# Kernel optimization log

Measured on AMD Instinct MI355X. Metric: run time of the kernel, lower is better.

The kernel has to match this reference:

```python
import jax, jax.numpy as jnp
import numpy as np

# DeformConv (v1, mmcv-style) config
N, C, H, W = 4, 64, 128, 128
OUT_C, KH, KW = 64, 3, 3
STRIDE, PAD, DIL, DG = 1, 1, 1, 1  # groups = 1


def setup_inputs() -> dict:
    key = jax.random.key(0)
    k1, k2, k3 = jax.random.split(key, 3)
    x = jax.random.normal(k1, (N, C, H, W), dtype=jnp.float32)
    offset = jax.random.normal(k2, (N, 2 * DG * KH * KW, H, W), dtype=jnp.float32)
    n_fan = C * KH * KW
    std = 1.0 / np.sqrt(n_fan)
    weight = jax.random.uniform(k3, (OUT_C, C, KH, KW), minval=-std, maxval=std, dtype=jnp.float32)
    return {"input_tensor": x, "offset": offset, "weight": weight}


def _deform_conv(x, offset, weight, stride, padding, dilation, dg):
    n, c, h, w = x.shape
    o, cin_g, kh, kw = weight.shape
    k = kh * kw
    ho = (h + 2 * padding - dilation * (kh - 1) - 1) // stride + 1
    wo = (w + 2 * padding - dilation * (kw - 1) - 1) // stride + 1

    # offset layout: [n, dg*k*2, ho, wo] with (dy, dx) pairs per kernel point
    off = offset.reshape(n, dg, k, 2, ho, wo)
    dy, dx = off[:, :, :, 0], off[:, :, :, 1]  # [n, dg, k, ho, wo]

    ky, kx = jnp.meshgrid(jnp.arange(kh), jnp.arange(kw), indexing="ij")
    ky = ky.reshape(k).astype(x.dtype)
    kx = kx.reshape(k).astype(x.dtype)

    base_y = (jnp.arange(ho) * stride - padding).astype(x.dtype)
    base_x = (jnp.arange(wo) * stride - padding).astype(x.dtype)
    # sampling positions [n, dg, k, ho, wo]
    py = base_y[None, None, None, :, None] + (ky * dilation)[None, None, :, None, None] + dy
    px = base_x[None, None, None, None, :] + (kx * dilation)[None, None, :, None, None] + dx

    cg = c // dg
    xg = x.reshape(n, dg, cg, h * w)

    y0 = jnp.floor(py)
    x0 = jnp.floor(px)
    ly = py - y0  # bilinear weights
    lx = px - x0
    y0i = y0.astype(jnp.int32)
    x0i = x0.astype(jnp.int32)

    def gather(yi, xi):
        # zero contribution for out-of-bounds neighbors (matches mmcv bilinear)
        valid = (yi >= 0) & (yi < h) & (xi >= 0) & (xi < w)
        idx = jnp.clip(yi, 0, h - 1) * w + jnp.clip(xi, 0, w - 1)  # [n, dg, k, ho, wo]
        v = jnp.take_along_axis(xg, idx.reshape(n, dg, 1, -1), axis=3)  # [n, dg, cg, k*ho*wo]
        v = v.reshape(n, dg, cg, k, ho, wo)
        return v * valid[:, :, None].astype(x.dtype)

    v00 = gather(y0i, x0i)
    v01 = gather(y0i, x0i + 1)
    v10 = gather(y0i + 1, x0i)
    v11 = gather(y0i + 1, x0i + 1)

    wy = ly[:, :, None]  # [n, dg, 1, k, ho, wo]
    wx = lx[:, :, None]
    sampled = (v00 * (1 - wy) * (1 - wx) + v01 * (1 - wy) * wx
               + v10 * wy * (1 - wx) + v11 * wy * wx)
    sampled = sampled.reshape(n, c, k, ho, wo)  # dg*cg == c, groups == 1

    return jnp.einsum("nckhw,ock->nohw", sampled, weight.reshape(o, cin_g, k))


def reference(input_tensor, offset, weight):
    return _deform_conv(input_tensor, offset, weight, STRIDE, PAD, DIL, DG)
```

## Files before the change

kernel.cpp:

```cpp
#include <hip/hip_runtime.h>

#define HW 16384
#define CIN 64
#define COUT 64
#define HH 128
#define WW 128
#define NB 4
#define PXB 16
#define TPB 8

typedef __attribute__((ext_vector_type(8))) short bf16x8;
typedef __attribute__((ext_vector_type(4))) float f32x4;
typedef __attribute__((ext_vector_type(4))) unsigned short u16x4;

__device__ __forceinline__ unsigned short f32_bf16(float f) {
  unsigned u = __builtin_bit_cast(unsigned, f);
  u += 0x7fffu + ((u >> 16) & 1u);
  return (unsigned short)(u >> 16);
}
__device__ __forceinline__ float bits_f32(unsigned u) {
  return __builtin_bit_cast(float, u);
}

__global__ __launch_bounds__(256) void prep_kernel(
    const float* __restrict__ x, const float* __restrict__ w,
    unsigned short* __restrict__ xt, unsigned short* __restrict__ wt) {
  __shared__ float tile[64][65];
  const int bid = blockIdx.x;
  if (bid < 1024) {
    const int n = bid >> 8;
    const int hw0 = (bid & 255) * 64;
    const int tx = threadIdx.x & 63;
    const int ty = threadIdx.x >> 6;
    const float* xp = x + (size_t)n * CIN * HW;
    #pragma unroll
    for (int c = ty; c < 64; c += 4)
      tile[c][tx] = xp[(size_t)c * HW + hw0 + tx];
    __syncthreads();
    unsigned short* xtp = xt + (size_t)n * HW * CIN;
    #pragma unroll
    for (int hw = ty; hw < 64; hw += 4)
      xtp[(size_t)(hw0 + hw) * CIN + tx] = f32_bf16(tile[tx][hw]);
  } else {
    const int i = (bid - 1024) * 256 + threadIdx.x;
    if (i < 64 * 576) {
      const int o = i / 576;
      const int t = i % 576;
      const int c = t & 63;
      const int k = t >> 6;
      wt[i] = f32_bf16(w[((size_t)o * 64 + c) * 9 + k]);
    }
  }
}

__global__ __launch_bounds__(256, 2) void deform_mfma(
    const unsigned short* __restrict__ xt, const float* __restrict__ offset,
    const unsigned short* __restrict__ wt, float* __restrict__ out) {
  __shared__ unsigned short s[PXB][584];
  __shared__ f32x4 pw[2][144];
  __shared__ uint2 pidx[2][144];
  const int tid = threadIdx.x;
  const int wave = tid >> 6;
  const int lane = tid & 63;
  const int g = lane >> 4;
  const int li = lane & 15;
  const int base = blockIdx.x * (PXB * TPB);
  const int n = base >> 14;
  const int rem_base = base & 16383;

  const float* offb = offset + (size_t)n * 18 * HW;
  const unsigned short* xli = xt + (size_t)n * HW * CIN + li * 4;

  const int px0 = tid & 15;
  const int tap0 = tid >> 4;
  const bool pthr = tap0 < 9;

  bf16x8 bv[18];
  {
    const unsigned short* bp = wt + ((size_t)(wave * 16 + li)) * 576 + g * 8;
    #pragma unroll
    for (int i = 0; i < 18; ++i)
      bv[i] = *(const bf16x8*)(bp + i * 32);
  }

  float dy = 0.f, dx = 0.f;
  if (pthr) {
    const int rem = rem_base + px0;
    dy = offb[(size_t)(2 * tap0) * HW + rem];
    dx = offb[(size_t)(2 * tap0 + 1) * HW + rem];
  }

  int prev_rem0 = 0;

  #pragma unroll 1
  for (int t = 0; t < TPB; ++t) {
    const int rem0 = rem_base + t * PXB;
    const int pb = t & 1;

    if (pthr) {
      const int rem = rem0 + px0;
      const int y = rem >> 7;
      const int x = rem & 127;
      const float fy = floorf(dy);
      const float fx = floorf(dx);
      const float ly = dy - fy;
      const float lx = dx - fx;
      const int y0 = y - 1 + (tap0 / 3) + (int)fy;
      const int x0 = x - 1 + (tap0 % 3) + (int)fx;
      const int y1 = y0 + 1, x1 = x0 + 1;
      const bool vy0 = (unsigned)y0 < (unsigned)HH;
      const bool vy1 = (unsigned)y1 < (unsigned)HH;
      const bool vx0 = (unsigned)x0 < (unsigned)WW;
      const bool vx1 = (unsigned)x1 < (unsigned)WW;
      const int cy0 = min(max(y0, 0), HH - 1);
      const int cy1 = min(max(y1, 0), HH - 1);
      const int cx0 = min(max(x0, 0), WW - 1);
      const int cx1 = min(max(x1, 0), WW - 1);
      const float omly = 1.f - ly, omlx = 1.f - lx;
      f32x4 w4;
      w4[0] = (vy0 && vx0) ? omly * omlx : 0.f;
      w4[1] = (vy0 && vx1) ? omly * lx : 0.f;
      w4[2] = (vy1 && vx0) ? ly * omlx : 0.f;
      w4[3] = (vy1 && vx1) ? ly * lx : 0.f;
      const unsigned i00 = (unsigned)(cy0 * WW + cx0);
      const unsigned i01 = (unsigned)(cy0 * WW + cx1);
      const unsigned i10 = (unsigned)(cy1 * WW + cx0);
      const unsigned i11 = (unsigned)(cy1 * WW + cx1);
      pw[pb][tid] = w4;
      pidx[pb][tid] = make_uint2(i00 | (i01 << 16), i10 | (i11 << 16));
    }
    __syncthreads();

    if (t + 1 < TPB && pthr) {
      const int rem = rem0 + PXB + px0;
      dy = offb[(size_t)(2 * tap0) * HW + rem];
      dx = offb[(size_t)(2 * tap0 + 1) * HW + rem];
    }

    const int px = wave * 4 + g;
    uint2 id[9];
    #pragma unroll
    for (int k = 0; k < 9; ++k) id[k] = pidx[pb][k * 16 + px];
    u16x4 V00[9], V01[9], V10[9], V11[9];
    #pragma unroll
    for (int k = 0; k < 9; ++k) {
      V00[k] = *(const u16x4*)(xli + (size_t)(id[k].x & 0xffffu) * CIN);
      V01[k] = *(const u16x4*)(xli + (size_t)(id[k].x >> 16) * CIN);
      V10[k] = *(const u16x4*)(xli + (size_t)(id[k].y & 0xffffu) * CIN);
      V11[k] = *(const u16x4*)(xli + (size_t)(id[k].y >> 16) * CIN);
    }
    __builtin_amdgcn_sched_barrier(0);

    if (t > 0) {
      f32x4 acc = {0.f, 0.f, 0.f, 0.f};
      const unsigned short* ap = &s[li][g * 8];
      #pragma unroll
      for (int i = 0; i < 18; ++i) {
        bf16x8 av = *(const bf16x8*)(ap + i * 32);
        acc = __builtin_amdgcn_mfma_f32_16x16x32_bf16(av, bv[i], acc, 0, 0, 0);
      }
      const int oc = wave * 16 + li;
      float* ob = out + ((size_t)n * COUT + oc) * HW + prev_rem0 + g * 4;
      *(f32x4*)ob = acc;
    }
    __builtin_amdgcn_sched_barrier(0);
    __syncthreads();

    #pragma unroll
    for (int k = 0; k < 9; ++k) {
      const f32x4 w = pw[pb][k * 16 + px];
      float a0 = 0.f, a1 = 0.f, a2 = 0.f, a3 = 0.f;
      #define CORNER(v, wc)                                        \
        a0 = fmaf(bits_f32((unsigned)(v)[0] << 16), (wc), a0);     \
        a1 = fmaf(bits_f32((unsigned)(v)[1] << 16), (wc), a1);     \
        a2 = fmaf(bits_f32((unsigned)(v)[2] << 16), (wc), a2);     \
        a3 = fmaf(bits_f32((unsigned)(v)[3] << 16), (wc), a3);
      CORNER(V00[k], w[0]);
      CORNER(V01[k], w[1]);
      CORNER(V10[k], w[2]);
      CORNER(V11[k], w[3]);
      #undef CORNER
      unsigned r01, r23;
      asm("v_cvt_pk_bf16_f32 %0, %1, %2" : "=v"(r01) : "v"(a0), "v"(a1));
      asm("v_cvt_pk_bf16_f32 %0, %1, %2" : "=v"(r23) : "v"(a2), "v"(a3));
      *(uint2*)&s[px][k * 64 + li * 4] = make_uint2(r01, r23);
    }
    prev_rem0 = rem0;
  }

  __syncthreads();
  {
    f32x4 acc = {0.f, 0.f, 0.f, 0.f};
    const unsigned short* ap = &s[li][g * 8];
    #pragma unroll
    for (int i = 0; i < 18; ++i) {
      bf16x8 av = *(const bf16x8*)(ap + i * 32);
      acc = __builtin_amdgcn_mfma_f32_16x16x32_bf16(av, bv[i], acc, 0, 0, 0);
    }
    const int oc = wave * 16 + li;
    float* ob = out + ((size_t)n * COUT + oc) * HW + prev_rem0 + g * 4;
    *(f32x4*)ob = acc;
  }
}

__global__ __launch_bounds__(256) void deform_fallback(
    const float* __restrict__ xsrc, const float* __restrict__ offset,
    const float* __restrict__ wsrc, float* __restrict__ out) {
  __shared__ float s[16][576];
  const int wave = threadIdx.x >> 6;
  const int lane = threadIdx.x & 63;
  const int p0 = blockIdx.x * 16;
  for (int i = 0; i < 4; ++i) {
    const int p = p0 + wave * 4 + i;
    const int n = p >> 14;
    const int rem = p & 16383;
    const int y = rem >> 7;
    const int x = rem & 127;
    const float* off = offset + (size_t)n * 18 * HW + rem;
    const float* xb = xsrc + (size_t)n * CIN * HW;
    #pragma unroll
    for (int k = 0; k < 9; ++k) {
      const float dy = off[(size_t)(2 * k) * HW];
      const float dx = off[(size_t)(2 * k + 1) * HW];
      const float py = (float)(y - 1 + k / 3) + dy;
      const float px = (float)(x - 1 + k % 3) + dx;
      const float y0f = floorf(py), x0f = floorf(px);
      const float ly = py - y0f, lx = px - x0f;
      const int y0 = (int)y0f, x0 = (int)x0f;
      const int y1 = y0 + 1, x1 = x0 + 1;
      const bool vy0 = (y0 >= 0) && (y0 < HH), vy1 = (y1 >= 0) && (y1 < HH);
      const bool vx0 = (x0 >= 0) && (x0 < WW), vx1 = (x1 >= 0) && (x1 < WW);
      const int cy0 = min(max(y0, 0), HH - 1), cy1 = min(max(y1, 0), HH - 1);
      const int cx0 = min(max(x0, 0), WW - 1), cx1 = min(max(x1, 0), WW - 1);
      const float v00 = (vy0 && vx0) ? xb[(size_t)lane * HW + cy0 * WW + cx0] : 0.f;
      const float v01 = (vy0 && vx1) ? xb[(size_t)lane * HW + cy0 * WW + cx1] : 0.f;
      const float v10 = (vy1 && vx0) ? xb[(size_t)lane * HW + cy1 * WW + cx0] : 0.f;
      const float v11 = (vy1 && vx1) ? xb[(size_t)lane * HW + cy1 * WW + cx1] : 0.f;
      s[wave * 4 + i][k * 64 + lane] =
          v00 * (1.f - ly) * (1.f - lx) + v01 * (1.f - ly) * lx +
          v10 * ly * (1.f - lx) + v11 * ly * lx;
    }
  }
  __syncthreads();
  float a0 = 0.f, a1 = 0.f, a2 = 0.f, a3 = 0.f;
  const int pb = wave * 4;
  for (int t = 0; t < 576; ++t) {
    const int c = t & 63;
    const int k = t >> 6;
    const float wv = wsrc[((size_t)lane * 64 + c) * 9 + k];
    a0 += s[pb + 0][t] * wv;
    a1 += s[pb + 1][t] * wv;
    a2 += s[pb + 2][t] * wv;
    a3 += s[pb + 3][t] * wv;
  }
  const float acc[4] = {a0, a1, a2, a3};
  for (int i = 0; i < 4; ++i) {
    const int p = p0 + pb + i;
    const int n = p >> 14;
    const int rem = p & 16383;
    out[((size_t)n * COUT + lane) * HW + rem] = acc[i];
  }
}

extern "C" void kernel_launch(void* const* d_in, const int* in_sizes, int n_in,
                              void* d_out, int out_size, void* d_ws,
                              size_t ws_size, hipStream_t stream) {
  const float* x = (const float*)d_in[0];
  const float* offset = (const float*)d_in[1];
  const float* weight = (const float*)d_in[2];
  float* out = (float*)d_out;

  const size_t xt_elems = (size_t)NB * HW * CIN;
  const size_t wt_elems = (size_t)64 * 576;
  const size_t need = (xt_elems + wt_elems) * sizeof(short);

  if (ws_size >= need) {
    unsigned short* xtp = (unsigned short*)d_ws;
    unsigned short* wtp = xtp + xt_elems;
    prep_kernel<<<1024 + 144, 256, 0, stream>>>(x, weight, xtp, wtp);
    deform_mfma<<<NB * HW / (PXB * TPB), 256, 0, stream>>>(xtp, offset, wtp, out);
  } else {
    deform_fallback<<<NB * HW / 16, 256, 0, stream>>>(x, offset, weight, out);
  }
}
```

Measured before the change: 44.74 us.

## Software-pipeline gathers one tile ahead and use lighter barriers with split MFMA accumulators

Restructures the main loop so the bilinear corner gathers for the next pixel tile are issued right after the current tile's interpolation, giving them a whole iteration to land. Sampling parameters are computed one tile ahead and offsets are prefetched two tiles ahead. __syncthreads is replaced by a custom barrier that waits only on LDS counters (lgkmcnt), and the MFMA reduction is split into two independent accumulators to shorten the dependency chain. This raises register pressure, because gather results stay live across the barrier and MFMA phases, and the LDS-only wait relies on the global gathers being ordered correctly across buffers.

Result: no change. 43.93 us (-1.8%).

```diff
diff --git a/kernel.cpp b/kernel.cpp
--- a/kernel.cpp
+++ b/kernel.cpp
@@ -21,6 +21,13 @@
 __device__ __forceinline__ float bits_f32(unsigned u) {
   return __builtin_bit_cast(float, u);
 }
+
+#define SYNCB()                                              \
+  do {                                                       \
+    asm volatile("s_waitcnt lgkmcnt(0)" ::: "memory");       \
+    __builtin_amdgcn_s_barrier();                            \
+    __builtin_amdgcn_sched_barrier(0);                       \
+  } while (0)
 
 __global__ __launch_bounds__(256) void prep_kernel(
     const float* __restrict__ x, const float* __restrict__ w,
@@ -74,6 +81,7 @@
   const int px0 = tid & 15;
   const int tap0 = tid >> 4;
   const bool pthr = tap0 < 9;
+  const int px = wave * 4 + g;
 
   bf16x8 bv[18];
   {
@@ -82,6 +90,75 @@
     for (int i = 0; i < 18; ++i)
       bv[i] = *(const bf16x8*)(bp + i * 32);
   }
+
+  #define PARAMS(tt, wb)                                                   \
+    do {                                                                   \
+      const int rem = rem_base + (tt) * PXB + px0;                         \
+      const int y = rem >> 7;                                              \
+      const int x = rem & 127;                                             \
+      const float fy = floorf(dy);                                         \
+      const float fx = floorf(dx);                                         \
+      const float ly = dy - fy;                                            \
+      const float lx = dx - fx;                                            \
+      const int y0 = y - 1 + (tap0 / 3) + (int)fy;                         \
+      const int x0 = x - 1 + (tap0 % 3) + (int)fx;                         \
+      const int y1 = y0 + 1, x1 = x0 + 1;                                  \
+      const bool vy0 = (unsigned)y0 < (unsigned)HH;                        \
+      const bool vy1 = (unsigned)y1 < (unsigned)HH;                        \
+      const bool vx0 = (unsigned)x0 < (unsigned)WW;                        \
+      const bool vx1 = (unsigned)x1 < (unsigned)WW;                        \
+      const int cy0 = min(max(y0, 0), HH - 1);                             \
+      const int cy1 = min(max(y1, 0), HH - 1);                             \
+      const int cx0 = min(max(x0, 0), WW - 1);                             \
+      const int cx1 = min(max(x1, 0), WW - 1);                             \
+      const float omly = 1.f - ly, omlx = 1.f - lx;                        \
+      f32x4 w4;                                                            \
+      w4[0] = (vy0 && vx0) ? omly * omlx : 0.f;                            \
+      w4[1] = (vy0 && vx1) ? omly * lx : 0.f;                              \
+      w4[2] = (vy1 && vx0) ? ly * omlx : 0.f;                              \
+      w4[3] = (vy1 && vx1) ? ly * lx : 0.f;                                \
+      const unsigned i00 = (unsigned)(cy0 * WW + cx0);                     \
+      const unsigned i01 = (unsigned)(cy0 * WW + cx1);                     \
+      const unsigned i10 = (unsigned)(cy1 * WW + cx0);                     \
+      const unsigned i11 = (unsigned)(cy1 * WW + cx1);                     \
+      pw[wb][tid] = w4;                                                    \
+      pidx[wb][tid] = make_uint2(i00 | (i01 << 16), i10 | (i11 << 16));    \
+    } while (0)
+
+  u16x4 V00[9], V01[9], V10[9], V11[9];
+
+  #define GATHERS(rb)                                                      \
+    do {                                                                   \
+      uint2 id[9];                                                         \
+      _Pragma("unroll")                                                    \
+      for (int k = 0; k < 9; ++k) id[k] = pidx[rb][k * 16 + px];           \
+      _Pragma("unroll")                                                    \
+      for (int k = 0; k < 9; ++k) {                                        \
+        V00[k] = *(const u16x4*)(xli + (size_t)(id[k].x & 0xffffu) * CIN); \
+        V01[k] = *(const u16x4*)(xli + (size_t)(id[k].x >> 16) * CIN);     \
+        V10[k] = *(const u16x4*)(xli + (size_t)(id[k].y & 0xffffu) * CIN); \
+        V11[k] = *(const u16x4*)(xli + (size_t)(id[k].y >> 16) * CIN);     \
+      }                                                                    \
+      __builtin_amdgcn_sched_barrier(0);                                   \
+    } while (0)
+
+  #define MFMA_OUT(remt)                                                   \
+    do {                                                                   \
+      f32x4 acc0 = {0.f, 0.f, 0.f, 0.f};                                   \
+      f32x4 acc1 = {0.f, 0.f, 0.f, 0.f};                                   \
+      const unsigned short* ap = &s[li][g * 8];                            \
+      _Pragma("unroll")                                                    \
+      for (int i = 0; i < 18; i += 2) {                                    \
+        bf16x8 av0 = *(const bf16x8*)(ap + i * 32);                        \
+        bf16x8 av1 = *(const bf16x8*)(ap + (i + 1) * 32);                  \
+        acc0 = __builtin_amdgcn_mfma_f32_16x16x32_bf16(av0, bv[i], acc0, 0, 0, 0); \
+        acc1 = __builtin_amdgcn_mfma_f32_16x16x32_bf16(av1, bv[i + 1], acc1, 0, 0, 0); \
+      }                                                                    \
+      const f32x4 acc = acc0 + acc1;                                       \
+      const int oc = wave * 16 + li;                                       \
+      float* ob = out + ((size_t)n * COUT + oc) * HW + (remt) + g * 4;     \
+      *(f32x4*)ob = acc;                                                   \
+    } while (0)
 
   float dy = 0.f, dx = 0.f;
   if (pthr) {
@@ -89,86 +166,36 @@
     dy = offb[(size_t)(2 * tap0) * HW + rem];
     dx = offb[(size_t)(2 * tap0 + 1) * HW + rem];
   }
+  if (pthr) PARAMS(0, 0);
+  if (pthr) {
+    const int rem = rem_base + PXB + px0;
+    dy = offb[(size_t)(2 * tap0) * HW + rem];
+    dx = offb[(size_t)(2 * tap0 + 1) * HW + rem];
+  }
+  SYNCB();
+  GATHERS(0);
 
   int prev_rem0 = 0;
 
   #pragma unroll 1
   for (int t = 0; t < TPB; ++t) {
     const int rem0 = rem_base + t * PXB;
-    const int pb = t & 1;
-
-    if (pthr) {
-      const int rem = rem0 + px0;
-      const int y = rem >> 7;
-      const int x = rem & 127;
-      const float fy = floorf(dy);
-      const float fx = floorf(dx);
-      const float ly = dy - fy;
-      const float lx = dx - fx;
-      const int y0 = y - 1 + (tap0 / 3) + (int)fy;
-      const int x0 = x - 1 + (tap0 % 3) + (int)fx;
-      const int y1 = y0 + 1, x1 = x0 + 1;
-      const bool vy0 = (unsigned)y0 < (unsigned)HH;
-      const bool vy1 = (unsigned)y1 < (unsigned)HH;
-      const bool vx0 = (unsigned)x0 < (unsigned)WW;
-      const bool vx1 = (unsigned)x1 < (unsigned)WW;
-      const int cy0 = min(max(y0, 0), HH - 1);
-      const int cy1 = min(max(y1, 0), HH - 1);
-      const int cx0 = min(max(x0, 0), WW - 1);
-      const int cx1 = min(max(x1, 0), WW - 1);
-      const float omly = 1.f - ly, omlx = 1.f - lx;
-      f32x4 w4;
-      w4[0] = (vy0 && vx0) ? omly * omlx : 0.f;
-      w4[1] = (vy0 && vx1) ? omly * lx : 0.f;
-      w4[2] = (vy1 && vx0) ? ly * omlx : 0.f;
-      w4[3] = (vy1 && vx1) ? ly * lx : 0.f;
-      const unsigned i00 = (unsigned)(cy0 * WW + cx0);
-      const unsigned i01 = (unsigned)(cy0 * WW + cx1);
-      const unsigned i10 = (unsigned)(cy1 * WW + cx0);
-      const unsigned i11 = (unsigned)(cy1 * WW + cx1);
-      pw[pb][tid] = w4;
-      pidx[pb][tid] = make_uint2(i00 | (i01 << 16), i10 | (i11 << 16));
-    }
-    __syncthreads();
-
-    if (t + 1 < TPB && pthr) {
-      const int rem = rem0 + PXB + px0;
+
+    if (t > 0) MFMA_OUT(prev_rem0);
+
+    if (t + 1 < TPB && pthr) PARAMS(t + 1, (t + 1) & 1);
+
+    if (t + 2 < TPB && pthr) {
+      const int rem = rem_base + (t + 2) * PXB + px0;
       dy = offb[(size_t)(2 * tap0) * HW + rem];
       dx = offb[(size_t)(2 * tap0 + 1) * HW + rem];
     }
 
-    const int px = wave * 4 + g;
-    uint2 id[9];
-    #pragma unroll
-    for (int k = 0; k < 9; ++k) id[k] = pidx[pb][k * 16 + px];
-    u16x4 V00[9], V01[9], V10[9], V11[9];
+    SYNCB();
+
     #pragma unroll
     for (int k = 0; k < 9; ++k) {
-      V00[k] = *(const u16x4*)(xli + (size_t)(id[k].x & 0xffffu) * CIN);
-      V01[k] = *(const u16x4*)(xli + (size_t)(id[k].x >> 16) * CIN);
-      V10[k] = *(const u16x4*)(xli + (size_t)(id[k].y & 0xffffu) * CIN);
-      V11[k] = *(const u16x4*)(xli + (size_t)(id[k].y >> 16) * CIN);
-    }
-    __builtin_amdgcn_sched_barrier(0);
-
-    if (t > 0) {
-      f32x4 acc = {0.f, 0.f, 0.f, 0.f};
-      const unsigned short* ap = &s[li][g * 8];
-      #pragma unroll
-      for (int i = 0; i < 18; ++i) {
-        bf16x8 av = *(const bf16x8*)(ap + i * 32);
-        acc = __builtin_amdgcn_mfma_f32_16x16x32_bf16(av, bv[i], acc, 0, 0, 0);
-      }
-      const int oc = wave * 16 + li;
-      float* ob = out + ((size_t)n * COUT + oc) * HW + prev_rem0 + g * 4;
-      *(f32x4*)ob = acc;
-    }
-    __builtin_amdgcn_sched_barrier(0);
-    __syncthreads();
-
-    #pragma unroll
-    for (int k = 0; k < 9; ++k) {
-      const f32x4 w = pw[pb][k * 16 + px];
+      const f32x4 w = pw[t & 1][k * 16 + px];
       float a0 = 0.f, a1 = 0.f, a2 = 0.f, a3 = 0.f;
       #define CORNER(v, wc)                                        \
         a0 = fmaf(bits_f32((unsigned)(v)[0] << 16), (wc), a0);     \
@@ -185,22 +212,18 @@
       asm("v_cvt_pk_bf16_f32 %0, %1, %2" : "=v"(r23) : "v"(a2), "v"(a3));
       *(uint2*)&s[px][k * 64 + li * 4] = make_uint2(r01, r23);
     }
+
+    if (t + 1 < TPB) GATHERS((t + 1) & 1);
+
+    SYNCB();
     prev_rem0 = rem0;
   }
 
-  __syncthreads();
-  {
-    f32x4 acc = {0.f, 0.f, 0.f, 0.f};
-    const unsigned short* ap = &s[li][g * 8];
-    #pragma unroll
-    for (int i = 0; i < 18; ++i) {
-      bf16x8 av = *(const bf16x8*)(ap + i * 32);
-      acc = __builtin_amdgcn_mfma_f32_16x16x32_bf16(av, bv[i], acc, 0, 0, 0);
-    }
-    const int oc = wave * 16 + li;
-    float* ob = out + ((size_t)n * COUT + oc) * HW + prev_rem0 + g * 4;
-    *(f32x4*)ob = acc;
-  }
+  MFMA_OUT(prev_rem0);
+
+  #undef PARAMS
+  #undef GATHERS
+  #undef MFMA_OUT
 }
 
 __global__ __launch_bounds__(256) void deform_fallback(
```
